# Performance work log

Hardware: AMD Instinct MI355X
Metric: run time of the kernel (lower is better)

The kernel has to match this reference:

```python
import jax, jax.numpy as jnp
import numpy as np

B, S, H = 4, 512, 1024
E, K, I = 8, 2, 2048

def setup_inputs() -> dict:
    key = jax.random.key(0)
    k1, k2, k3, k4, k5 = jax.random.split(key, 5)
    scale_h = 1.0 / np.sqrt(H)
    scale_i = 1.0 / np.sqrt(I)
    return {
        "hidden_states": jax.random.normal(k1, (B, S, H), dtype=jnp.float32),
        "router_w": jax.random.normal(k2, (E, H), dtype=jnp.float32) * scale_h,
        "w_gate": jax.random.normal(k3, (E, H, I), dtype=jnp.float32) * scale_h,
        "w_up": jax.random.normal(k4, (E, H, I), dtype=jnp.float32) * scale_h,
        "w_down": jax.random.normal(k5, (E, I, H), dtype=jnp.float32) * scale_i,
    }

def reference(hidden_states, router_w, w_gate, w_up, w_down):
    b, s, h = hidden_states.shape
    x = hidden_states.reshape(-1, h)              # [T, H] tokens
    T = x.shape[0]

    # ---- RouterTopK: fp32 linear -> softmax over all experts -> top-k ----
    router_logits = x.astype(jnp.float32) @ router_w.T          # [T, E]
    probs = jax.nn.softmax(router_logits, axis=-1)               # [T, E]
    top_vals, top_idx = jax.lax.top_k(probs, K)                  # [T, K]

    # normalize_top_k_affinities (norm_topk_prob=True)
    top_vals = top_vals / jnp.sum(top_vals, axis=-1, keepdims=True)

    # scatter normalized affinities into a dense [T, E] combine matrix
    aff = jnp.zeros((T, E), dtype=x.dtype).at[jnp.arange(T)[:, None], top_idx].set(top_vals.astype(x.dtype))

    # ---- ExpertMLPs: GLU (swiglu) per expert, combine weighted by affinity ----
    # Dense-per-expert computation; non-selected experts contribute 0 via aff.
    gate = jnp.einsum('th,ehi->eti', x, w_gate)                  # [E, T, I]
    up = jnp.einsum('th,ehi->eti', x, w_up)                      # [E, T, I]
    act = jax.nn.silu(gate) * up                                 # [E, T, I]
    expert_out = jnp.einsum('eti,eih->eth', act, w_down)         # [E, T, H]
    out = jnp.einsum('eth,te->th', expert_out, aff)              # [T, H]

    # _reduce_output: all-reduce over TP/world group -> identity single-device
    return out.reshape(b, s, h)
```

## Files before the change

### kernel.cpp

```cpp
#include <hip/hip_runtime.h>
#include <hip/hip_bf16.h>

#define T_TOK 2048
#define H_DIM 1024
#define E_N   8
#define I_DIM 2048

#define NT_MAX 40
#define MAX_SLOTS 5120

typedef unsigned short u16;
typedef unsigned int   u32;
typedef __bf16 bf16_t;
typedef bf16_t bf16x8 __attribute__((ext_vector_type(8)));
typedef u16    u16x8  __attribute__((ext_vector_type(8)));
typedef float  f32x4  __attribute__((ext_vector_type(4)));

#define MFMA __builtin_amdgcn_mfma_f32_16x16x32_bf16

__device__ __forceinline__ u16 bfbits(float f) {
    bf16_t b = (bf16_t)f;
    return __builtin_bit_cast(u16, b);
}

__device__ __forceinline__ void gload_lds16(const void* g, void* l) {
    __builtin_amdgcn_global_load_lds(
        (const __attribute__((address_space(1))) void*)g,
        (__attribute__((address_space(3))) void*)l, 16, 0, 0);
}

__device__ __forceinline__ int tile_off(int n, int kb) {
    return n * 64 + ((kb ^ ((n >> 1) & 7)) << 3);
}
__device__ __forceinline__ int a_off(int row, int kslot) {
    return row * 64 + ((kslot ^ (row & 7)) << 3);
}

__global__ __launch_bounds__(256) void router_k(
    const float* __restrict__ x, const float* __restrict__ rw,
    int* __restrict__ cnt, int* __restrict__ tok, float* __restrict__ wts,
    u16* __restrict__ xbf)
{
    int wid = threadIdx.x >> 6, lane = threadIdx.x & 63;
    int t = blockIdx.x * 4 + wid;
    const float* xr = x + (size_t)t * H_DIM;
    u16* xbr = xbf + (size_t)t * H_DIM;

    float acc[E_N];
#pragma unroll
    for (int e = 0; e < E_N; e++) acc[e] = 0.f;
    for (int j = 0; j < H_DIM / 64; j++) {
        float xv = xr[lane + 64 * j];
        xbr[lane + 64 * j] = bfbits(xv);
#pragma unroll
        for (int e = 0; e < E_N; e++)
            acc[e] += xv * rw[e * H_DIM + lane + 64 * j];
    }
#pragma unroll
    for (int e = 0; e < E_N; e++) {
        float v = acc[e];
        for (int off = 32; off; off >>= 1) v += __shfl_xor(v, off);
        acc[e] = v;
    }
    if (lane == 0) {
        int i0 = 0; float m0 = acc[0];
#pragma unroll
        for (int e = 1; e < E_N; e++) if (acc[e] > m0) { m0 = acc[e]; i0 = e; }
        int i1 = -1; float m1 = -INFINITY;
#pragma unroll
        for (int e = 0; e < E_N; e++) if (e != i0 && acc[e] > m1) { m1 = acc[e]; i1 = e; }
        float w0 = 1.f / (1.f + expf(m1 - m0));
        float w1 = 1.f - w0;
        int p0 = atomicAdd(&cnt[i0], 1);
        tok[i0 * T_TOK + p0] = t; wts[i0 * T_TOK + p0] = w0;
        int p1 = atomicAdd(&cnt[i1], 1);
        tok[i1 * T_TOK + p1] = t; wts[i1 * T_TOK + p1] = w1;
    }
}

__global__ void prefix_k(const int* __restrict__ cnt, int* __restrict__ offs_pad,
                         int* __restrict__ tile_e, int* __restrict__ tile_row0,
                         int* __restrict__ ntiles)
{
    if (threadIdx.x == 0) {
        int s = 0, nt = 0;
        for (int e = 0; e < E_N; e++) {
            offs_pad[e] = s;
            int c = cnt[e];
            int t = (c + 127) >> 7;
            for (int i = 0; i < t; i++) { tile_e[nt] = e; tile_row0[nt] = i * 128; nt++; }
            s += t * 128;
        }
        offs_pad[E_N] = s;
        *ntiles = nt;
    }
}

__global__ __launch_bounds__(512, 2) void gateup_k(
    const u16* __restrict__ xbf, const float* __restrict__ wg, const float* __restrict__ wu,
    const int* __restrict__ cnt, const int* __restrict__ offs_pad,
    const int* __restrict__ tile_e, const int* __restrict__ tile_row0,
    const int* __restrict__ ntiles, const int* __restrict__ tok,
    u16* __restrict__ act)
{
    int q = gridDim.x >> 3;
    int phys = blockIdx.x;
    int logical = (phys & 7) * q + (phys >> 3);
    int tb = logical % NT_MAX;
    int p  = logical / NT_MAX;
    if (tb >= *ntiles) return;
    int e = tile_e[tb], row0 = tile_row0[tb];
    int cntE = cnt[e];
    int slot0 = offs_pad[e] + row0;
    int n0 = p * 128;

    __shared__ u16 AS[2][8192], GS[2][8192], US[2][8192];

    int tid = threadIdx.x;
    int lane = tid & 63, wid = tid >> 6;
    int wm = wid & 3, wn = wid >> 2;
    int l15 = lane & 15, lg = lane >> 4;

    const u16* asrc[2];
#pragma unroll
    for (int i = 0; i < 2; i++) {
        int row = (wid * 2 + i) * 8 + (lane >> 3);
        int rc = (row0 + row < cntE) ? (row0 + row) : (cntE - 1);
        asrc[i] = xbf + (size_t)tok[e * T_TOK + rc] * H_DIM + (((lane & 7) ^ (lane >> 3)) << 3);
    }
    int s0 = wid * 1024;

    int bn = tid & 127;
    int kq = tid >> 7;
    const float* gsrc = wg + (size_t)e * H_DIM * I_DIM + n0 + bn;
    const float* usrc = wu + (size_t)e * H_DIM * I_DIM + n0 + bn;

    float g0[16], u0[16], g1[16], u1[16];

#define BLOAD(gs, us, t) { \
    _Pragma("unroll") \
    for (int j = 0; j < 16; j++) { \
        gs[j] = gsrc[(size_t)((t) * 64 + kq * 16 + j) * I_DIM]; \
        us[j] = usrc[(size_t)((t) * 64 + kq * 16 + j) * I_DIM]; } }

#define BWRITE(gs, us, nbuf) { \
    _Pragma("unroll") \
    for (int jb = 0; jb < 2; jb++) { \
        u16x8 pg, pu; \
        _Pragma("unroll") \
        for (int jj = 0; jj < 8; jj++) { pg[jj] = bfbits(gs[jb * 8 + jj]); pu[jj] = bfbits(us[jb * 8 + jj]); } \
        *reinterpret_cast<u16x8*>(&GS[nbuf][tile_off(bn, kq * 2 + jb)]) = pg; \
        *reinterpret_cast<u16x8*>(&US[nbuf][tile_off(bn, kq * 2 + jb)]) = pu; } }

#define ASTAGE(nbuf, t) { \
    gload_lds16(asrc[0] + (size_t)(t) * 64, &AS[nbuf][s0]); \
    gload_lds16(asrc[1] + (size_t)(t) * 64, &AS[nbuf][s0 + 512]); }

    f32x4 accg[2][4], accu[2][4];
#pragma unroll
    for (int a = 0; a < 2; a++)
#pragma unroll
        for (int b = 0; b < 4; b++) { accg[a][b] = (f32x4)0.f; accu[a][b] = (f32x4)0.f; }

#define CLUSTER(bufi) { \
    _Pragma("unroll") \
    for (int ks = 0; ks < 2; ks++) { \
        bf16x8 af[2]; \
        _Pragma("unroll") \
        for (int mf = 0; mf < 2; mf++) { \
            int row = wm * 32 + mf * 16 + l15; \
            af[mf] = *reinterpret_cast<const bf16x8*>(&AS[bufi][a_off(row, ks * 4 + lg)]); } \
        int kbr = ks * 4 + lg; \
        _Pragma("unroll") \
        for (int nf = 0; nf < 4; nf++) { \
            int c = wn * 64 + nf * 16 + l15; \
            int o = tile_off(c, kbr); \
            bf16x8 bg = *reinterpret_cast<const bf16x8*>(&GS[bufi][o]); \
            bf16x8 bu = *reinterpret_cast<const bf16x8*>(&US[bufi][o]); \
            _Pragma("unroll") \
            for (int mf = 0; mf < 2; mf++) { \
                accg[mf][nf] = MFMA(af[mf], bg, accg[mf][nf], 0, 0, 0); \
                accu[mf][nf] = MFMA(af[mf], bu, accu[mf][nf], 0, 0, 0); } } } }

    ASTAGE(0, 0);
    __builtin_amdgcn_sched_barrier(0);
    BLOAD(g0, u0, 0);
    __builtin_amdgcn_sched_barrier(0);
    BLOAD(g1, u1, 1);
    __builtin_amdgcn_sched_barrier(0);
    BWRITE(g0, u0, 0);
    __builtin_amdgcn_sched_barrier(0);
    asm volatile("s_waitcnt vmcnt(0) lgkmcnt(0)" ::: "memory");
    __builtin_amdgcn_s_barrier();
    __builtin_amdgcn_sched_barrier(0);

    for (int t2 = 0; t2 < 16; t2 += 2) {
        if (t2 + 1 < 16) ASTAGE(1, t2 + 1);
        CLUSTER(0);
        __builtin_amdgcn_sched_barrier(0);
        if (t2 + 1 < 16) BWRITE(g1, u1, 1);
        __builtin_amdgcn_sched_barrier(0);
        if (t2 + 2 < 16) {
            BLOAD(g0, u0, t2 + 2);
            __builtin_amdgcn_sched_barrier(0);
            asm volatile("s_waitcnt vmcnt(32) lgkmcnt(0)" ::: "memory");
        } else {
            asm volatile("s_waitcnt vmcnt(0) lgkmcnt(0)" ::: "memory");
        }
        __builtin_amdgcn_s_barrier();
        __builtin_amdgcn_sched_barrier(0);

        {
            int t = t2 + 1;
            if (t + 1 < 16) ASTAGE(0, t + 1);
            CLUSTER(1);
            __builtin_amdgcn_sched_barrier(0);
            if (t + 1 < 16) {
                BWRITE(g0, u0, 0);
                __builtin_amdgcn_sched_barrier(0);
                if (t + 2 < 16) {
                    BLOAD(g1, u1, t + 2);
                    __builtin_amdgcn_sched_barrier(0);
                    asm volatile("s_waitcnt vmcnt(32) lgkmcnt(0)" ::: "memory");
                } else {
                    asm volatile("s_waitcnt vmcnt(0) lgkmcnt(0)" ::: "memory");
                }
                __builtin_amdgcn_s_barrier();
                __builtin_amdgcn_sched_barrier(0);
            }
        }
    }
#undef BLOAD
#undef BWRITE
#undef ASTAGE
#undef CLUSTER

#pragma unroll
    for (int mf = 0; mf < 2; mf++)
#pragma unroll
        for (int j = 0; j < 4; j++) {
            int rl = wm * 32 + mf * 16 + lg * 4 + j;
            bool valid = (row0 + rl) < cntE;
            size_t base = (size_t)(slot0 + rl) * I_DIM + n0;
#pragma unroll
            for (int nf = 0; nf < 4; nf++) {
                float g = accg[mf][nf][j];
                float u = accu[mf][nf][j];
                float a = valid ? (g / (1.f + expf(-g))) * u : 0.f;
                act[base + wn * 64 + nf * 16 + l15] = bfbits(a);
            }
        }
}

__global__ __launch_bounds__(512, 4) void down_k(
    const u16* __restrict__ act, const float* __restrict__ wd,
    const int* __restrict__ cnt, const int* __restrict__ offs_pad,
    const int* __restrict__ tile_e, const int* __restrict__ tile_row0,
    const int* __restrict__ ntiles, const int* __restrict__ tok,
    const float* __restrict__ wts, float* __restrict__ out)
{
    int q = gridDim.x >> 3;
    int phys = blockIdx.x;
    int logical = (phys & 7) * q + (phys >> 3);
    int tb = logical % NT_MAX;
    int rest = logical / NT_MAX;
    int p  = rest & 7;
    int kh = rest >> 3;
    if (tb >= *ntiles) return;
    int e = tile_e[tb], row0 = tile_row0[tb];
    int cntE = cnt[e];
    int slot0 = offs_pad[e] + row0;
    int h0 = p * 128;

    __shared__ u16 AS[2][8192], DS[2][8192];

    int tid = threadIdx.x;
    int lane = tid & 63, wid = tid >> 6;
    int wm = wid & 3, wn = wid >> 2;
    int l15 = lane & 15, lg = lane >> 4;

    const u16* asrc[2];
#pragma unroll
    for (int i = 0; i < 2; i++) {
        int row = (wid * 2 + i) * 8 + (lane >> 3);
        asrc[i] = act + (size_t)(slot0 + row) * I_DIM + kh * 1024
                  + (((lane & 7) ^ (lane >> 3)) << 3);
    }
    int s0 = wid * 1024;

    int bn = tid & 127;
    int kq = tid >> 7;
    const float* dsrc = wd + ((size_t)e * I_DIM + kh * 1024) * H_DIM + h0 + bn;

    float v0[16], v1[16];

#define BLOAD(vs, t) { \
    _Pragma("unroll") \
    for (int j = 0; j < 16; j++) \
        vs[j] = dsrc[(size_t)((t) * 64 + kq * 16 + j) * H_DIM]; }

#define BWRITE(vs, nbuf) { \
    _Pragma("unroll") \
    for (int jb = 0; jb < 2; jb++) { \
        u16x8 pk; \
        _Pragma("unroll") \
        for (int jj = 0; jj < 8; jj++) pk[jj] = bfbits(vs[jb * 8 + jj]); \
        *reinterpret_cast<u16x8*>(&DS[nbuf][tile_off(bn, kq * 2 + jb)]) = pk; } }

#define ASTAGE(nbuf, t) { \
    gload_lds16(asrc[0] + (size_t)(t) * 64, &AS[nbuf][s0]); \
    gload_lds16(asrc[1] + (size_t)(t) * 64, &AS[nbuf][s0 + 512]); }

    f32x4 acc[2][4];
#pragma unroll
    for (int a = 0; a < 2; a++)
#pragma unroll
        for (int b = 0; b < 4; b++) acc[a][b] = (f32x4)0.f;

#define CLUSTER(bufi) { \
    _Pragma("unroll") \
    for (int ks = 0; ks < 2; ks++) { \
        bf16x8 af[2]; \
        _Pragma("unroll") \
        for (int mf = 0; mf < 2; mf++) { \
            int row = wm * 32 + mf * 16 + l15; \
            af[mf] = *reinterpret_cast<const bf16x8*>(&AS[bufi][a_off(row, ks * 4 + lg)]); } \
        int kbr = ks * 4 + lg; \
        _Pragma("unroll") \
        for (int nf = 0; nf < 4; nf++) { \
            int c = wn * 64 + nf * 16 + l15; \
            bf16x8 bd = *reinterpret_cast<const bf16x8*>(&DS[bufi][tile_off(c, kbr)]); \
            _Pragma("unroll") \
            for (int mf = 0; mf < 2; mf++) \
                acc[mf][nf] = MFMA(af[mf], bd, acc[mf][nf], 0, 0, 0); } } }

    ASTAGE(0, 0);
    __builtin_amdgcn_sched_barrier(0);
    BLOAD(v0, 0);
    __builtin_amdgcn_sched_barrier(0);
    BLOAD(v1, 1);
    __builtin_amdgcn_sched_barrier(0);
    BWRITE(v0, 0);
    __builtin_amdgcn_sched_barrier(0);
    asm volatile("s_waitcnt vmcnt(0) lgkmcnt(0)" ::: "memory");
    __builtin_amdgcn_s_barrier();
    __builtin_amdgcn_sched_barrier(0);

    for (int t2 = 0; t2 < 16; t2 += 2) {
        if (t2 + 1 < 16) ASTAGE(1, t2 + 1);
        CLUSTER(0);
        __builtin_amdgcn_sched_barrier(0);
        if (t2 + 1 < 16) BWRITE(v1, 1);
        __builtin_amdgcn_sched_barrier(0);
        if (t2 + 2 < 16) {
            BLOAD(v0, t2 + 2);
            __builtin_amdgcn_sched_barrier(0);
            asm volatile("s_waitcnt vmcnt(16) lgkmcnt(0)" ::: "memory");
        } else {
            asm volatile("s_waitcnt vmcnt(0) lgkmcnt(0)" ::: "memory");
        }
        __builtin_amdgcn_s_barrier();
        __builtin_amdgcn_sched_barrier(0);

        {
            int t = t2 + 1;
            if (t + 1 < 16) ASTAGE(0, t + 1);
            CLUSTER(1);
            __builtin_amdgcn_sched_barrier(0);
            if (t + 1 < 16) {
                BWRITE(v0, 0);
                __builtin_amdgcn_sched_barrier(0);
                if (t + 2 < 16) {
                    BLOAD(v1, t + 2);
                    __builtin_amdgcn_sched_barrier(0);
                    asm volatile("s_waitcnt vmcnt(16) lgkmcnt(0)" ::: "memory");
                } else {
                    asm volatile("s_waitcnt vmcnt(0) lgkmcnt(0)" ::: "memory");
                }
                __builtin_amdgcn_s_barrier();
                __builtin_amdgcn_sched_barrier(0);
            }
        }
    }
#undef BLOAD
#undef BWRITE
#undef ASTAGE
#undef CLUSTER

#pragma unroll
    for (int mf = 0; mf < 2; mf++)
#pragma unroll
        for (int j = 0; j < 4; j++) {
            int rl = wm * 32 + mf * 16 + lg * 4 + j;
            int gr = row0 + rl;
            if (gr < cntE) {
                float w = wts[e * T_TOK + gr];
                int t   = tok[e * T_TOK + gr];
                size_t base = (size_t)t * H_DIM + h0;
#pragma unroll
                for (int nf = 0; nf < 4; nf++)
                    atomicAdd(&out[base + wn * 64 + nf * 16 + l15], acc[mf][nf][j] * w);
            }
        }
}

extern "C" void kernel_launch(void* const* d_in, const int* in_sizes, int n_in,
                              void* d_out, int out_size, void* d_ws, size_t ws_size,
                              hipStream_t stream)
{
    const float* x  = (const float*)d_in[0];
    const float* rw = (const float*)d_in[1];
    const float* wg = (const float*)d_in[2];
    const float* wu = (const float*)d_in[3];
    const float* wd = (const float*)d_in[4];
    float* out = (float*)d_out;

    char* ws = (char*)d_ws;
    int*   cnt       = (int*)(ws);
    int*   ntiles    = (int*)(ws + 32);
    int*   offs_pad  = (int*)(ws + 64);
    int*   tile_e    = (int*)(ws + 256);
    int*   tile_row0 = (int*)(ws + 512);
    int*   tok       = (int*)(ws + 64 * 1024);
    float* wts       = (float*)(ws + 128 * 1024);
    u16*   xbf       = (u16*)(ws + 256 * 1024);
    u16*   act       = (u16*)(ws + 4608 * 1024);

    size_t need = 4608ull * 1024 + (size_t)MAX_SLOTS * I_DIM * 2;
    if (ws_size < need) return;

    hipMemsetAsync(cnt, 0, 32, stream);
    hipMemsetAsync(out, 0, (size_t)T_TOK * H_DIM * sizeof(float), stream);

    router_k<<<T_TOK / 4, 256, 0, stream>>>(x, rw, cnt, tok, wts, xbf);
    prefix_k<<<1, 64, 0, stream>>>(cnt, offs_pad, tile_e, tile_row0, ntiles);
    gateup_k<<<NT_MAX * (I_DIM / 128), 512, 0, stream>>>(
        xbf, wg, wu, cnt, offs_pad, tile_e, tile_row0, ntiles, tok, act);
    down_k<<<NT_MAX * (H_DIM / 128) * 2, 512, 0, stream>>>(
        act, wd, cnt, offs_pad, tile_e, tile_row0, ntiles, tok, wts, out);
}
```

Measured before the change: 218.8 us.

## Split gate/up GEMM into two passes and switch to 32x32x16 MFMA tiles

Replaces the fused gate+up kernel with a templated kernel launched twice. The first pass writes the gate result to a bf16 scratch buffer, and the second computes up and applies SiLU while reading that buffer back. Both GEMM kernels move from 512-thread blocks using 16x16x32 MFMA to 256-thread blocks using 32x32x16 MFMA, with four waves each covering a 64x64 sub-tile. The aim is fewer LDS fragment reads per MFMA, lower register pressure and smaller LDS use. The cost is an extra kernel launch, a re-read of the activations, an extra bf16 round-trip of gate values through global memory, and more weight-load work per thread.

Result: slower. 294.2 us (+34.5%).

```diff
diff --git a/kernel.cpp b/kernel.cpp
--- a/kernel.cpp
+++ b/kernel.cpp
@@ -14,13 +14,17 @@
 typedef __bf16 bf16_t;
 typedef bf16_t bf16x8 __attribute__((ext_vector_type(8)));
 typedef u16    u16x8  __attribute__((ext_vector_type(8)));
-typedef float  f32x4  __attribute__((ext_vector_type(4)));
-
-#define MFMA __builtin_amdgcn_mfma_f32_16x16x32_bf16
+typedef float  f32x16 __attribute__((ext_vector_type(16)));
+
+#define MFMA32 __builtin_amdgcn_mfma_f32_32x32x16_bf16
 
 __device__ __forceinline__ u16 bfbits(float f) {
     bf16_t b = (bf16_t)f;
     return __builtin_bit_cast(u16, b);
+}
+__device__ __forceinline__ float bf2f(u16 u) {
+    u32 x = ((u32)u) << 16;
+    return __builtin_bit_cast(float, x);
 }
 
 __device__ __forceinline__ void gload_lds16(const void* g, void* l) {
@@ -96,12 +100,13 @@
     }
 }
 
-__global__ __launch_bounds__(512, 2) void gateup_k(
-    const u16* __restrict__ xbf, const float* __restrict__ wg, const float* __restrict__ wu,
+template <int MODE>
+__global__ __launch_bounds__(256, 2) void gu_k(
+    const u16* __restrict__ xbf, const float* __restrict__ W,
     const int* __restrict__ cnt, const int* __restrict__ offs_pad,
     const int* __restrict__ tile_e, const int* __restrict__ tile_row0,
     const int* __restrict__ ntiles, const int* __restrict__ tok,
-    u16* __restrict__ act)
+    u16* __restrict__ gbuf, u16* __restrict__ act)
 {
     int q = gridDim.x >> 3;
     int phys = blockIdx.x;
@@ -114,81 +119,76 @@
     int slot0 = offs_pad[e] + row0;
     int n0 = p * 128;
 
-    __shared__ u16 AS[2][8192], GS[2][8192], US[2][8192];
+    __shared__ u16 AS[2][8192], BS[2][8192];
 
     int tid = threadIdx.x;
     int lane = tid & 63, wid = tid >> 6;
-    int wm = wid & 3, wn = wid >> 2;
-    int l15 = lane & 15, lg = lane >> 4;
-
-    const u16* asrc[2];
-#pragma unroll
-    for (int i = 0; i < 2; i++) {
-        int row = (wid * 2 + i) * 8 + (lane >> 3);
+    int wm = wid >> 1, wn = wid & 1;
+    int l31 = lane & 31, lh = lane >> 5;
+
+    const u16* asrc[4];
+#pragma unroll
+    for (int i = 0; i < 4; i++) {
+        int row = (wid * 4 + i) * 8 + (lane >> 3);
         int rc = (row0 + row < cntE) ? (row0 + row) : (cntE - 1);
-        asrc[i] = xbf + (size_t)tok[e * T_TOK + rc] * H_DIM + (((lane & 7) ^ (lane >> 3)) << 3);
-    }
-    int s0 = wid * 1024;
+        asrc[i] = xbf + (size_t)tok[e * T_TOK + rc] * H_DIM
+                  + (((lane & 7) ^ ((lane >> 3) & 7)) << 3);
+    }
+    int s0 = wid * 2048;
 
     int bn = tid & 127;
-    int kq = tid >> 7;
-    const float* gsrc = wg + (size_t)e * H_DIM * I_DIM + n0 + bn;
-    const float* usrc = wu + (size_t)e * H_DIM * I_DIM + n0 + bn;
-
-    float g0[16], u0[16], g1[16], u1[16];
-
-#define BLOAD(gs, us, t) { \
-    _Pragma("unroll") \
-    for (int j = 0; j < 16; j++) { \
-        gs[j] = gsrc[(size_t)((t) * 64 + kq * 16 + j) * I_DIM]; \
-        us[j] = usrc[(size_t)((t) * 64 + kq * 16 + j) * I_DIM]; } }
-
-#define BWRITE(gs, us, nbuf) { \
-    _Pragma("unroll") \
-    for (int jb = 0; jb < 2; jb++) { \
-        u16x8 pg, pu; \
-        _Pragma("unroll") \
-        for (int jj = 0; jj < 8; jj++) { pg[jj] = bfbits(gs[jb * 8 + jj]); pu[jj] = bfbits(us[jb * 8 + jj]); } \
-        *reinterpret_cast<u16x8*>(&GS[nbuf][tile_off(bn, kq * 2 + jb)]) = pg; \
-        *reinterpret_cast<u16x8*>(&US[nbuf][tile_off(bn, kq * 2 + jb)]) = pu; } }
+    int khalf = tid >> 7;
+    const float* wsrc = W + (size_t)e * H_DIM * I_DIM + n0 + bn;
+
+    float v0[32], v1[32];
+
+#define BLOAD(vs, t) { \
+    _Pragma("unroll") \
+    for (int j = 0; j < 32; j++) \
+        vs[j] = wsrc[(size_t)((t) * 64 + khalf * 32 + j) * I_DIM]; }
+
+#define BWRITE(vs, nbuf) { \
+    _Pragma("unroll") \
+    for (int jb = 0; jb < 4; jb++) { \
+        u16x8 pk; \
+        _Pragma("unroll") \
+        for (int jj = 0; jj < 8; jj++) pk[jj] = bfbits(vs[jb * 8 + jj]); \
+        *reinterpret_cast<u16x8*>(&BS[nbuf][tile_off(bn, khalf * 4 + jb)]) = pk; } }
 
 #define ASTAGE(nbuf, t) { \
-    gload_lds16(asrc[0] + (size_t)(t) * 64, &AS[nbuf][s0]); \
-    gload_lds16(asrc[1] + (size_t)(t) * 64, &AS[nbuf][s0 + 512]); }
-
-    f32x4 accg[2][4], accu[2][4];
+    _Pragma("unroll") \
+    for (int i = 0; i < 4; i++) \
+        gload_lds16(asrc[i] + (size_t)(t) * 64, &AS[nbuf][s0 + i * 512]); }
+
+    f32x16 acc[2][2];
 #pragma unroll
     for (int a = 0; a < 2; a++)
 #pragma unroll
-        for (int b = 0; b < 4; b++) { accg[a][b] = (f32x4)0.f; accu[a][b] = (f32x4)0.f; }
+        for (int b = 0; b < 2; b++) acc[a][b] = (f32x16)0.f;
 
 #define CLUSTER(bufi) { \
     _Pragma("unroll") \
-    for (int ks = 0; ks < 2; ks++) { \
-        bf16x8 af[2]; \
-        _Pragma("unroll") \
-        for (int mf = 0; mf < 2; mf++) { \
-            int row = wm * 32 + mf * 16 + l15; \
-            af[mf] = *reinterpret_cast<const bf16x8*>(&AS[bufi][a_off(row, ks * 4 + lg)]); } \
-        int kbr = ks * 4 + lg; \
-        _Pragma("unroll") \
-        for (int nf = 0; nf < 4; nf++) { \
-            int c = wn * 64 + nf * 16 + l15; \
-            int o = tile_off(c, kbr); \
-            bf16x8 bg = *reinterpret_cast<const bf16x8*>(&GS[bufi][o]); \
-            bf16x8 bu = *reinterpret_cast<const bf16x8*>(&US[bufi][o]); \
+    for (int ks = 0; ks < 4; ks++) { \
+        bf16x8 af[2], bfr[2]; \
+        _Pragma("unroll") \
+        for (int mf = 0; mf < 2; mf++) \
+            af[mf] = *reinterpret_cast<const bf16x8*>(&AS[bufi][a_off(wm * 64 + mf * 32 + l31, ks * 2 + lh)]); \
+        _Pragma("unroll") \
+        for (int nf = 0; nf < 2; nf++) \
+            bfr[nf] = *reinterpret_cast<const bf16x8*>(&BS[bufi][tile_off(wn * 64 + nf * 32 + l31, ks * 2 + lh)]); \
+        _Pragma("unroll") \
+        for (int mf = 0; mf < 2; mf++) \
             _Pragma("unroll") \
-            for (int mf = 0; mf < 2; mf++) { \
-                accg[mf][nf] = MFMA(af[mf], bg, accg[mf][nf], 0, 0, 0); \
-                accu[mf][nf] = MFMA(af[mf], bu, accu[mf][nf], 0, 0, 0); } } } }
+            for (int nf = 0; nf < 2; nf++) \
+                acc[mf][nf] = MFMA32(af[mf], bfr[nf], acc[mf][nf], 0, 0, 0); } }
 
     ASTAGE(0, 0);
     __builtin_amdgcn_sched_barrier(0);
-    BLOAD(g0, u0, 0);
-    __builtin_amdgcn_sched_barrier(0);
-    BLOAD(g1, u1, 1);
-    __builtin_amdgcn_sched_barrier(0);
-    BWRITE(g0, u0, 0);
+    BLOAD(v0, 0);
+    __builtin_amdgcn_sched_barrier(0);
+    BLOAD(v1, 1);
+    __builtin_amdgcn_sched_barrier(0);
+    BWRITE(v0, 0);
     __builtin_amdgcn_sched_barrier(0);
     asm volatile("s_waitcnt vmcnt(0) lgkmcnt(0)" ::: "memory");
     __builtin_amdgcn_s_barrier();
@@ -198,10 +198,10 @@
         if (t2 + 1 < 16) ASTAGE(1, t2 + 1);
         CLUSTER(0);
         __builtin_amdgcn_sched_barrier(0);
-        if (t2 + 1 < 16) BWRITE(g1, u1, 1);
+        if (t2 + 1 < 16) BWRITE(v1, 1);
         __builtin_amdgcn_sched_barrier(0);
         if (t2 + 2 < 16) {
-            BLOAD(g0, u0, t2 + 2);
+            BLOAD(v0, t2 + 2);
             __builtin_amdgcn_sched_barrier(0);
             asm volatile("s_waitcnt vmcnt(32) lgkmcnt(0)" ::: "memory");
         } else {
@@ -216,10 +216,10 @@
             CLUSTER(1);
             __builtin_amdgcn_sched_barrier(0);
             if (t + 1 < 16) {
-                BWRITE(g0, u0, 0);
+                BWRITE(v0, 0);
                 __builtin_amdgcn_sched_barrier(0);
                 if (t + 2 < 16) {
-                    BLOAD(g1, u1, t + 2);
+                    BLOAD(v1, t + 2);
                     __builtin_amdgcn_sched_barrier(0);
                     asm volatile("s_waitcnt vmcnt(32) lgkmcnt(0)" ::: "memory");
                 } else {
@@ -238,21 +238,26 @@
 #pragma unroll
     for (int mf = 0; mf < 2; mf++)
 #pragma unroll
-        for (int j = 0; j < 4; j++) {
-            int rl = wm * 32 + mf * 16 + lg * 4 + j;
-            bool valid = (row0 + rl) < cntE;
-            size_t base = (size_t)(slot0 + rl) * I_DIM + n0;
-#pragma unroll
-            for (int nf = 0; nf < 4; nf++) {
-                float g = accg[mf][nf][j];
-                float u = accu[mf][nf][j];
-                float a = valid ? (g / (1.f + expf(-g))) * u : 0.f;
-                act[base + wn * 64 + nf * 16 + l15] = bfbits(a);
+        for (int nf = 0; nf < 2; nf++) {
+            int col = n0 + wn * 64 + nf * 32 + l31;
+#pragma unroll
+            for (int r = 0; r < 16; r++) {
+                int rl = wm * 64 + mf * 32 + (r & 3) + 8 * (r >> 2) + 4 * lh;
+                size_t idx = (size_t)(slot0 + rl) * I_DIM + col;
+                if constexpr (MODE == 0) {
+                    gbuf[idx] = bfbits(acc[mf][nf][r]);
+                } else {
+                    bool valid = (row0 + rl) < cntE;
+                    float g = bf2f(gbuf[idx]);
+                    float u = acc[mf][nf][r];
+                    float a = valid ? (g / (1.f + expf(-g))) * u : 0.f;
+                    act[idx] = bfbits(a);
+                }
             }
         }
 }
 
-__global__ __launch_bounds__(512, 4) void down_k(
+__global__ __launch_bounds__(256, 2) void down_k(
     const u16* __restrict__ act, const float* __restrict__ wd,
     const int* __restrict__ cnt, const int* __restrict__ offs_pad,
     const int* __restrict__ tile_e, const int* __restrict__ tile_row0,
@@ -272,67 +277,67 @@
     int slot0 = offs_pad[e] + row0;
     int h0 = p * 128;
 
-    __shared__ u16 AS[2][8192], DS[2][8192];
+    __shared__ u16 AS[2][8192], BS[2][8192];
 
     int tid = threadIdx.x;
     int lane = tid & 63, wid = tid >> 6;
-    int wm = wid & 3, wn = wid >> 2;
-    int l15 = lane & 15, lg = lane >> 4;
-
-    const u16* asrc[2];
-#pragma unroll
-    for (int i = 0; i < 2; i++) {
-        int row = (wid * 2 + i) * 8 + (lane >> 3);
+    int wm = wid >> 1, wn = wid & 1;
+    int l31 = lane & 31, lh = lane >> 5;
+
+    const u16* asrc[4];
+#pragma unroll
+    for (int i = 0; i < 4; i++) {
+        int row = (wid * 4 + i) * 8 + (lane >> 3);
         asrc[i] = act + (size_t)(slot0 + row) * I_DIM + kh * 1024
-                  + (((lane & 7) ^ (lane >> 3)) << 3);
-    }
-    int s0 = wid * 1024;
+                  + (((lane & 7) ^ ((lane >> 3) & 7)) << 3);
+    }
+    int s0 = wid * 2048;
 
     int bn = tid & 127;
-    int kq = tid >> 7;
+    int khalf = tid >> 7;
     const float* dsrc = wd + ((size_t)e * I_DIM + kh * 1024) * H_DIM + h0 + bn;
 
-    float v0[16], v1[16];
+    float v0[32], v1[32];
 
 #define BLOAD(vs, t) { \
     _Pragma("unroll") \
-    for (int j = 0; j < 16; j++) \
-        vs[j] = dsrc[(size_t)((t) * 64 + kq * 16 + j) * H_DIM]; }
+    for (int j = 0; j < 32; j++) \
+        vs[j] = dsrc[(size_t)((t) * 64 + khalf * 32 + j) * H_DIM]; }
 
 #define BWRITE(vs, nbuf) { \
     _Pragma("unroll") \
-    for (int jb = 0; jb < 2; jb++) { \
+    for (int jb = 0; jb < 4; jb++) { \
         u16x8 pk; \
         _Pragma("unroll") \
         for (int jj = 0; jj < 8; jj++) pk[jj] = bfbits(vs[jb * 8 + jj]); \
-        *reinterpret_cast<u16x8*>(&DS[nbuf][tile_off(bn, kq * 2 + jb)]) = pk; } }
+        *reinterpret_cast<u16x8*>(&BS[nbuf][tile_off(bn, khalf * 4 + jb)]) = pk; } }
 
 #define ASTAGE(nbuf, t) { \
-    gload_lds16(asrc[0] + (size_t)(t) * 64, &AS[nbuf][s0]); \
-    gload_lds16(asrc[1] + (size_t)(t) * 64, &AS[nbuf][s0 + 512]); }
-
-    f32x4 acc[2][4];
+    _Pragma("unroll") \
+    for (int i = 0; i < 4; i++) \
+        gload_lds16(asrc[i] + (size_t)(t) * 64, &AS[nbuf][s0 + i * 512]); }
+
+    f32x16 acc[2][2];
 #pragma unroll
     for (int a = 0; a < 2; a++)
 #pragma unroll
-        for (int b = 0; b < 4; b++) acc[a][b] = (f32x4)0.f;
+        for (int b = 0; b < 2; b++) acc[a][b] = (f32x16)0.f;
 
 #define CLUSTER(bufi) { \
     _Pragma("unroll") \
-    for (int ks = 0; ks < 2; ks++) { \
-        bf16x8 af[2]; \
-        _Pragma("unroll") \
-        for (int mf = 0; mf < 2; mf++) { \
-            int row = wm * 32 + mf * 16 + l15; \
-            af[mf] = *reinterpret_cast<const bf16x8*>(&AS[bufi][a_off(row, ks * 4 + lg)]); } \
-        int kbr = ks * 4 + lg; \
-        _Pragma("unroll") \
-        for (int nf = 0; nf < 4; nf++) { \
-            int c = wn * 64 + nf * 16 + l15; \
-            bf16x8 bd = *reinterpret_cast<const bf16x8*>(&DS[bufi][tile_off(c, kbr)]); \
+    for (int ks = 0; ks < 4; ks++) { \
+        bf16x8 af[2], bfr[2]; \
+        _Pragma("unroll") \
+        for (int mf = 0; mf < 2; mf++) \
+            af[mf] = *reinterpret_cast<const bf16x8*>(&AS[bufi][a_off(wm * 64 + mf * 32 + l31, ks * 2 + lh)]); \
+        _Pragma("unroll") \
+        for (int nf = 0; nf < 2; nf++) \
+            bfr[nf] = *reinterpret_cast<const bf16x8*>(&BS[bufi][tile_off(wn * 64 + nf * 32 + l31, ks * 2 + lh)]); \
+        _Pragma("unroll") \
+        for (int mf = 0; mf < 2; mf++) \
             _Pragma("unroll") \
-            for (int mf = 0; mf < 2; mf++) \
-                acc[mf][nf] = MFMA(af[mf], bd, acc[mf][nf], 0, 0, 0); } } }
+            for (int nf = 0; nf < 2; nf++) \
+                acc[mf][nf] = MFMA32(af[mf], bfr[nf], acc[mf][nf], 0, 0, 0); } }
 
     ASTAGE(0, 0);
     __builtin_amdgcn_sched_barrier(0);
@@ -355,7 +360,7 @@
         if (t2 + 2 < 16) {
             BLOAD(v0, t2 + 2);
             __builtin_amdgcn_sched_barrier(0);
-            asm volatile("s_waitcnt vmcnt(16) lgkmcnt(0)" ::: "memory");
+            asm volatile("s_waitcnt vmcnt(32) lgkmcnt(0)" ::: "memory");
         } else {
             asm volatile("s_waitcnt vmcnt(0) lgkmcnt(0)" ::: "memory");
         }
@@ -373,7 +378,7 @@
                 if (t + 2 < 16) {
                     BLOAD(v1, t + 2);
                     __builtin_amdgcn_sched_barrier(0);
-                    asm volatile("s_waitcnt vmcnt(16) lgkmcnt(0)" ::: "memory");
+                    asm volatile("s_waitcnt vmcnt(32) lgkmcnt(0)" ::: "memory");
                 } else {
                     asm volatile("s_waitcnt vmcnt(0) lgkmcnt(0)" ::: "memory");
                 }
@@ -390,16 +395,17 @@
 #pragma unroll
     for (int mf = 0; mf < 2; mf++)
 #pragma unroll
-        for (int j = 0; j < 4; j++) {
-            int rl = wm * 32 + mf * 16 + lg * 4 + j;
-            int gr = row0 + rl;
-            if (gr < cntE) {
-                float w = wts[e * T_TOK + gr];
-                int t   = tok[e * T_TOK + gr];
-                size_t base = (size_t)t * H_DIM + h0;
-#pragma unroll
-                for (int nf = 0; nf < 4; nf++)
-                    atomicAdd(&out[base + wn * 64 + nf * 16 + l15], acc[mf][nf][j] * w);
+        for (int nf = 0; nf < 2; nf++) {
+            int col = h0 + wn * 64 + nf * 32 + l31;
+#pragma unroll
+            for (int r = 0; r < 16; r++) {
+                int rl = wm * 64 + mf * 32 + (r & 3) + 8 * (r >> 2) + 4 * lh;
+                int gr = row0 + rl;
+                if (gr < cntE) {
+                    float w = wts[e * T_TOK + gr];
+                    int t   = tok[e * T_TOK + gr];
+                    atomicAdd(&out[(size_t)t * H_DIM + col], acc[mf][nf][r] * w);
+                }
             }
         }
 }
@@ -425,8 +431,9 @@
     float* wts       = (float*)(ws + 128 * 1024);
     u16*   xbf       = (u16*)(ws + 256 * 1024);
     u16*   act       = (u16*)(ws + 4608 * 1024);
-
-    size_t need = 4608ull * 1024 + (size_t)MAX_SLOTS * I_DIM * 2;
+    u16*   gbuf      = (u16*)(ws + 26ull * 1024 * 1024);
+
+    size_t need = 26ull * 1024 * 1024 + (size_t)MAX_SLOTS * I_DIM * 2;
     if (ws_size < need) return;
 
     hipMemsetAsync(cnt, 0, 32, stream);
@@ -434,8 +441,10 @@
 
     router_k<<<T_TOK / 4, 256, 0, stream>>>(x, rw, cnt, tok, wts, xbf);
     prefix_k<<<1, 64, 0, stream>>>(cnt, offs_pad, tile_e, tile_row0, ntiles);
-    gateup_k<<<NT_MAX * (I_DIM / 128), 512, 0, stream>>>(
-        xbf, wg, wu, cnt, offs_pad, tile_e, tile_row0, ntiles, tok, act);
-    down_k<<<NT_MAX * (H_DIM / 128) * 2, 512, 0, stream>>>(
+    gu_k<0><<<NT_MAX * (I_DIM / 128), 256, 0, stream>>>(
+        xbf, wg, cnt, offs_pad, tile_e, tile_row0, ntiles, tok, gbuf, act);
+    gu_k<1><<<NT_MAX * (I_DIM / 128), 256, 0, stream>>>(
+        xbf, wu, cnt, offs_pad, tile_e, tile_row0, ntiles, tok, gbuf, act);
+    down_k<<<NT_MAX * (H_DIM / 128) * 2, 256, 0, stream>>>(
         act, wd, cnt, offs_pad, tile_e, tile_row0, ntiles, tok, wts, out);
 }
```
